# Performance work log

Hardware: AMD Instinct MI355X
Metric: run time of the kernel (lower is better)

The kernel has to match this reference:

```python
import jax, jax.numpy as jnp
import numpy as np

H0, H1, NHID, BATCH = 256, 256, 512, 2048

def setup_inputs() -> dict:
    key = jax.random.key(0)
    k1, k2, k3, k4, k5 = jax.random.split(key, 5)
    initrange = 0.1
    inputs = jax.random.normal(k1, (BATCH, NHID), dtype=jnp.float32)
    labels = jax.random.randint(k2, (BATCH,), 0, H1, dtype=jnp.int32)
    parent_labels = jax.random.randint(k3, (BATCH,), 0, H0, dtype=jnp.int32)
    layer_top_W = jax.random.uniform(k4, (NHID, H0), jnp.float32, -initrange, initrange)
    layer_top_b = jnp.zeros((H0,), jnp.float32)
    layer_bottom_W = jax.random.uniform(k5, (H0, NHID, H1), jnp.float32, -initrange, initrange)
    layer_bottom_b = jnp.zeros((H0, H1), jnp.float32)
    return {"inputs": inputs, "labels": labels, "parent_labels": parent_labels,
            "layer_top_W": layer_top_W, "layer_top_b": layer_top_b,
            "layer_bottom_W": layer_bottom_W, "layer_bottom_b": layer_bottom_b}

def reference(inputs, labels, parent_labels, layer_top_W, layer_top_b,
              layer_bottom_W, layer_bottom_b):
    batch = inputs.shape[0]
    # top-level softmax over coarse classes: [B, H0]
    top_probs = jax.nn.softmax(inputs @ layer_top_W + layer_top_b, axis=1)
    # per-sample gather of expert weight slice [B, NHID, H1] then bmm
    Wb = layer_bottom_W[parent_labels]            # [B, NHID, H1]
    bb = layer_bottom_b[parent_labels]            # [B, H1]
    bottom_logits = jnp.einsum('bd,bdk->bk', inputs, Wb) + bb
    bottom_probs = jax.nn.softmax(bottom_logits, axis=1)
    ar = jnp.arange(batch)
    target_probs = top_probs[ar, parent_labels] * bottom_probs[ar, labels]
    return target_probs
```

## Files before the change

### kernel.cpp

```cpp
#include <hip/hip_runtime.h>

constexpr int BATCH = 2048;
constexpr int NHID  = 512;
constexpr int H0    = 256;
constexpr int H1    = 256;
constexpr int S     = 8;
constexpr int J     = 3;

__global__ __launch_bounds__(128) void hs_8s(
    const float* __restrict__ x,
    const int*   __restrict__ labels,
    const int*   __restrict__ parents,
    const float* __restrict__ topW,
    const float* __restrict__ topb,
    const float* __restrict__ botW,
    const float* __restrict__ botb,
    float*       __restrict__ out)
{
    const int p = blockIdx.x / J;
    const int j = blockIdx.x % J;
    const int t = threadIdx.x;
    const int g = t >> 6;
    const int l = t & 63;

    __shared__ int   list[BATCH];
    __shared__ int   wcnt[2];
    __shared__ __align__(16) float xs[S][NHID];
    __shared__ float psm[2][S];

    int running = 0;
    for (int c = 0; c < BATCH; c += 128) {
        const bool match = (parents[c + t] == p);
        const unsigned long long mask = __ballot(match);
        if (l == 0) wcnt[g] = __popcll(mask);
        __syncthreads();
        const int off = running + (g ? wcnt[0] : 0);
        if (match)
            list[off + __popcll(mask & ((1ull << l) - 1ull))] = c + t;
        running += wcnt[0] + wcnt[1];
        __syncthreads();
    }
    const int n = running;
    if (n <= j * S) return;

    const float* Wbase = g ? botW + (size_t)p * NHID * H1 : topW;
    const float4 b4    = g ? *(const float4*)(botb + (size_t)p * H1 + 4 * l)
                           : *(const float4*)(topb + 4 * l);

    for (int base = j * S; base < n; base += J * S) {
        const int rem = min(S, n - base);

        for (int s = 0; s < S; ++s) {
            const int idx = list[base + min(s, rem - 1)];
            ((float4*)xs[s])[t] = ((const float4*)(x + (size_t)idx * NHID))[t];
        }

        int tgts[S];
        #pragma unroll
        for (int s = 0; s < S; ++s) {
            const int slot = base + min(s, rem - 1);
            tgts[s] = g ? labels[list[slot]] : p;
        }
        __syncthreads();

        float4 acc[S];
        #pragma unroll
        for (int s = 0; s < S; ++s) acc[s] = make_float4(0.f, 0.f, 0.f, 0.f);

        const float* Wp = Wbase + 4 * l;
        float4 ring[8];
        #pragma unroll
        for (int i = 0; i < 8; ++i)
            ring[i] = *(const float4*)(Wp + (size_t)i * H0);

        for (int d = 0; d < NHID; d += 8) {
            #pragma unroll
            for (int h = 0; h < 2; ++h) {
                const int dd = d + 4 * h;
                const float4 w0 = ring[4 * h + 0], w1 = ring[4 * h + 1];
                const float4 w2 = ring[4 * h + 2], w3 = ring[4 * h + 3];
                if (dd + 8 < NHID) {
                    #pragma unroll
                    for (int i = 0; i < 4; ++i)
                        ring[4 * h + i] =
                            *(const float4*)(Wp + (size_t)(dd + 8 + i) * H0);
                }
                #pragma unroll
                for (int s = 0; s < S; ++s) {
                    const float4 xv = *(const float4*)&xs[s][dd];
                    float4 a = acc[s];
                    a.x = fmaf(xv.x, w0.x, a.x); a.y = fmaf(xv.x, w0.y, a.y);
                    a.z = fmaf(xv.x, w0.z, a.z); a.w = fmaf(xv.x, w0.w, a.w);
                    a.x = fmaf(xv.y, w1.x, a.x); a.y = fmaf(xv.y, w1.y, a.y);
                    a.z = fmaf(xv.y, w1.z, a.z); a.w = fmaf(xv.y, w1.w, a.w);
                    a.x = fmaf(xv.z, w2.x, a.x); a.y = fmaf(xv.z, w2.y, a.y);
                    a.z = fmaf(xv.z, w2.z, a.z); a.w = fmaf(xv.z, w2.w, a.w);
                    a.x = fmaf(xv.w, w3.x, a.x); a.y = fmaf(xv.w, w3.y, a.y);
                    a.z = fmaf(xv.w, w3.z, a.z); a.w = fmaf(xv.w, w3.w, a.w);
                    acc[s] = a;
                }
            }
        }

        #pragma unroll
        for (int s = 0; s < S; ++s) {
            float4 v = acc[s];
            v.x += b4.x; v.y += b4.y; v.z += b4.z; v.w += b4.w;

            float m = fmaxf(fmaxf(v.x, v.y), fmaxf(v.z, v.w));
            #pragma unroll
            for (int off = 32; off > 0; off >>= 1)
                m = fmaxf(m, __shfl_xor(m, off, 64));

            const float ex = expf(v.x - m), ey = expf(v.y - m);
            const float ez = expf(v.z - m), ew = expf(v.w - m);
            float sum = (ex + ey) + (ez + ew);
            #pragma unroll
            for (int off = 32; off > 0; off >>= 1)
                sum += __shfl_xor(sum, off, 64);

            const int tgt = tgts[s];
            const int k   = tgt & 3;
            const float ev = (k == 0) ? ex : (k == 1) ? ey : (k == 2) ? ez : ew;
            if (l == (tgt >> 2))
                psm[g][s] = ev / sum;
        }
        __syncthreads();

        if (t < rem) {
            const int idx = list[base + t];
            out[idx] = psm[0][t] * psm[1][t];
        }
        __syncthreads();
    }
}

extern "C" void kernel_launch(void* const* d_in, const int* in_sizes, int n_in,
                              void* d_out, int out_size, void* d_ws, size_t ws_size,
                              hipStream_t stream) {
    const float* x       = (const float*)d_in[0];
    const int*   labels  = (const int*)  d_in[1];
    const int*   parents = (const int*)  d_in[2];
    const float* topW    = (const float*)d_in[3];
    const float* topb    = (const float*)d_in[4];
    const float* botW    = (const float*)d_in[5];
    const float* botb    = (const float*)d_in[6];
    float*       out     = (float*)d_out;

    hs_8s<<<H0 * J, 128, 0, stream>>>(x, labels, parents,
                                      topW, topb, botW, botb, out);
}
```

Baseline: 227.9 us.

## Split output columns across two waves per pass with cross-wave softmax merge

Each block now runs 256 threads: four waves, where each of the top and bottom passes is split across two waves covering 128 output columns each (float2 per lane). Samples per tile rise to 12 and the per-parent split drops from 3 to 2 blocks, so each block re-reads its expert weight slice fewer times in total. Partial max, sum and target-exp values from the two halves are merged in shared memory with a rescaled log-sum-exp. This trades fewer weight re-reads for less per-thread work and more per-wave FMA parallelism, at the cost of extra shuffles, an additional target reduction and more registers for the 12-sample accumulators.

Result: slower. 286.1 us (+25.6%).

```diff
diff --git a/kernel.cpp b/kernel.cpp
--- a/kernel.cpp
+++ b/kernel.cpp
@@ -4,10 +4,10 @@
 constexpr int NHID  = 512;
 constexpr int H0    = 256;
 constexpr int H1    = 256;
-constexpr int S     = 8;
-constexpr int J     = 3;
+constexpr int S     = 12;
+constexpr int NSLOT = 2;
 
-__global__ __launch_bounds__(128) void hs_8s(
+__global__ __launch_bounds__(256) void hs_minbytes(
     const float* __restrict__ x,
     const int*   __restrict__ labels,
     const int*   __restrict__ parents,
@@ -17,119 +17,136 @@
     const float* __restrict__ botb,
     float*       __restrict__ out)
 {
-    const int p = blockIdx.x / J;
-    const int j = blockIdx.x % J;
-    const int t = threadIdx.x;
-    const int g = t >> 6;
-    const int l = t & 63;
+    const int p    = blockIdx.x >> 1;
+    const int slot = blockIdx.x & 1;
+    const int t    = threadIdx.x;
+    const int gb   = t >> 6;
+    const int l    = t & 63;
+    const int mypass = gb >> 1;
+    const int h      = gb & 1;
 
     __shared__ int   list[BATCH];
-    __shared__ int   wcnt[2];
+    __shared__ int   wcnt[4];
     __shared__ __align__(16) float xs[S][NHID];
-    __shared__ float psm[2][S];
+    __shared__ float wm[2][2][S], wsum[2][2][S], wet[2][2][S];
 
     int running = 0;
-    for (int c = 0; c < BATCH; c += 128) {
+    for (int c = 0; c < BATCH; c += 256) {
         const bool match = (parents[c + t] == p);
         const unsigned long long mask = __ballot(match);
-        if (l == 0) wcnt[g] = __popcll(mask);
+        if (l == 0) wcnt[gb] = __popcll(mask);
         __syncthreads();
-        const int off = running + (g ? wcnt[0] : 0);
+        int off = running;
+        for (int w = 0; w < gb; ++w) off += wcnt[w];
         if (match)
             list[off + __popcll(mask & ((1ull << l) - 1ull))] = c + t;
-        running += wcnt[0] + wcnt[1];
+        running += wcnt[0] + wcnt[1] + wcnt[2] + wcnt[3];
         __syncthreads();
     }
     const int n = running;
-    if (n <= j * S) return;
+    if (n <= slot * S) return;
 
-    const float* Wbase = g ? botW + (size_t)p * NHID * H1 : topW;
-    const float4 b4    = g ? *(const float4*)(botb + (size_t)p * H1 + 4 * l)
-                           : *(const float4*)(topb + 4 * l);
+    const float* Wbase = mypass ? botW + (size_t)p * NHID * H1 : topW;
+    const float* Wp    = Wbase + 128 * h + 2 * l;
+    const float2 b2    = mypass
+        ? *(const float2*)(botb + (size_t)p * H1 + 128 * h + 2 * l)
+        : *(const float2*)(topb + 128 * h + 2 * l);
+    const int c0 = 128 * h + 2 * l;
 
-    for (int base = j * S; base < n; base += J * S) {
+    for (int base = slot * S; base < n; base += NSLOT * S) {
         const int rem = min(S, n - base);
 
-        for (int s = 0; s < S; ++s) {
-            const int idx = list[base + min(s, rem - 1)];
-            ((float4*)xs[s])[t] = ((const float4*)(x + (size_t)idx * NHID))[t];
+        for (int pr = 0; pr < S / 2; ++pr) {
+            const int row = 2 * pr + (t >> 7);
+            const int col = t & 127;
+            const int idx = list[base + min(row, rem - 1)];
+            ((float4*)xs[row])[col] = ((const float4*)(x + (size_t)idx * NHID))[col];
         }
 
         int tgts[S];
         #pragma unroll
         for (int s = 0; s < S; ++s) {
-            const int slot = base + min(s, rem - 1);
-            tgts[s] = g ? labels[list[slot]] : p;
+            const int slotidx = base + min(s, rem - 1);
+            tgts[s] = mypass ? labels[list[slotidx]] : p;
         }
         __syncthreads();
 
-        float4 acc[S];
+        float2 acc[S];
         #pragma unroll
-        for (int s = 0; s < S; ++s) acc[s] = make_float4(0.f, 0.f, 0.f, 0.f);
+        for (int s = 0; s < S; ++s) acc[s] = make_float2(0.f, 0.f);
 
-        const float* Wp = Wbase + 4 * l;
-        float4 ring[8];
+        float2 ring[16];
         #pragma unroll
-        for (int i = 0; i < 8; ++i)
-            ring[i] = *(const float4*)(Wp + (size_t)i * H0);
+        for (int i = 0; i < 16; ++i)
+            ring[i] = *(const float2*)(Wp + (size_t)i * H0);
 
-        for (int d = 0; d < NHID; d += 8) {
+        #pragma unroll 4
+        for (int d4 = 0; d4 < NHID / 4; ++d4) {
+            const int rs = (d4 & 3) * 4;
+            const float2 w0 = ring[rs + 0], w1 = ring[rs + 1];
+            const float2 w2 = ring[rs + 2], w3 = ring[rs + 3];
+            const int dn = 4 * d4 + 16;
+            if (dn < NHID) {
+                #pragma unroll
+                for (int i = 0; i < 4; ++i)
+                    ring[rs + i] = *(const float2*)(Wp + (size_t)(dn + i) * H0);
+            }
+            const int d = 4 * d4;
             #pragma unroll
-            for (int h = 0; h < 2; ++h) {
-                const int dd = d + 4 * h;
-                const float4 w0 = ring[4 * h + 0], w1 = ring[4 * h + 1];
-                const float4 w2 = ring[4 * h + 2], w3 = ring[4 * h + 3];
-                if (dd + 8 < NHID) {
-                    #pragma unroll
-                    for (int i = 0; i < 4; ++i)
-                        ring[4 * h + i] =
-                            *(const float4*)(Wp + (size_t)(dd + 8 + i) * H0);
-                }
-                #pragma unroll
-                for (int s = 0; s < S; ++s) {
-                    const float4 xv = *(const float4*)&xs[s][dd];
-                    float4 a = acc[s];
-                    a.x = fmaf(xv.x, w0.x, a.x); a.y = fmaf(xv.x, w0.y, a.y);
-                    a.z = fmaf(xv.x, w0.z, a.z); a.w = fmaf(xv.x, w0.w, a.w);
-                    a.x = fmaf(xv.y, w1.x, a.x); a.y = fmaf(xv.y, w1.y, a.y);
-                    a.z = fmaf(xv.y, w1.z, a.z); a.w = fmaf(xv.y, w1.w, a.w);
-                    a.x = fmaf(xv.z, w2.x, a.x); a.y = fmaf(xv.z, w2.y, a.y);
-                    a.z = fmaf(xv.z, w2.z, a.z); a.w = fmaf(xv.z, w2.w, a.w);
-                    a.x = fmaf(xv.w, w3.x, a.x); a.y = fmaf(xv.w, w3.y, a.y);
-                    a.z = fmaf(xv.w, w3.z, a.z); a.w = fmaf(xv.w, w3.w, a.w);
-                    acc[s] = a;
-                }
+            for (int s = 0; s < S; ++s) {
+                const float4 xv = *(const float4*)&xs[s][d];
+                float2 a = acc[s];
+                a.x = fmaf(xv.x, w0.x, a.x);  a.y = fmaf(xv.x, w0.y, a.y);
+                a.x = fmaf(xv.y, w1.x, a.x);  a.y = fmaf(xv.y, w1.y, a.y);
+                a.x = fmaf(xv.z, w2.x, a.x);  a.y = fmaf(xv.z, w2.y, a.y);
+                a.x = fmaf(xv.w, w3.x, a.x);  a.y = fmaf(xv.w, w3.y, a.y);
+                acc[s] = a;
             }
         }
 
         #pragma unroll
         for (int s = 0; s < S; ++s) {
-            float4 v = acc[s];
-            v.x += b4.x; v.y += b4.y; v.z += b4.z; v.w += b4.w;
+            float2 v = acc[s];
+            v.x += b2.x; v.y += b2.y;
 
-            float m = fmaxf(fmaxf(v.x, v.y), fmaxf(v.z, v.w));
+            float m = fmaxf(v.x, v.y);
             #pragma unroll
             for (int off = 32; off > 0; off >>= 1)
                 m = fmaxf(m, __shfl_xor(m, off, 64));
 
-            const float ex = expf(v.x - m), ey = expf(v.y - m);
-            const float ez = expf(v.z - m), ew = expf(v.w - m);
-            float sum = (ex + ey) + (ez + ew);
+            const float ex = expf(v.x - m);
+            const float ey = expf(v.y - m);
+            float sum = ex + ey;
             #pragma unroll
             for (int off = 32; off > 0; off >>= 1)
                 sum += __shfl_xor(sum, off, 64);
 
             const int tgt = tgts[s];
-            const int k   = tgt & 3;
-            const float ev = (k == 0) ? ex : (k == 1) ? ey : (k == 2) ? ez : ew;
-            if (l == (tgt >> 2))
-                psm[g][s] = ev / sum;
+            float et = (c0 == tgt) ? ex : (c0 + 1 == tgt) ? ey : 0.f;
+            #pragma unroll
+            for (int off = 32; off > 0; off >>= 1)
+                et += __shfl_xor(et, off, 64);
+
+            if (l == 0) {
+                wm[mypass][h][s]   = m;
+                wsum[mypass][h][s] = sum;
+                wet[mypass][h][s]  = et;
+            }
         }
         __syncthreads();
 
         if (t < rem) {
-            const int idx = list[base + t];
-            out[idx] = psm[0][t] * psm[1][t];
+            float pr[2];
+            #pragma unroll
+            for (int ps = 0; ps < 2; ++ps) {
+                const float m0 = wm[ps][0][t], m1 = wm[ps][1][t];
+                const float m  = fmaxf(m0, m1);
+                const float a0 = expf(m0 - m), a1 = expf(m1 - m);
+                const float sum = wsum[ps][0][t] * a0 + wsum[ps][1][t] * a1;
+                const float et  = wet[ps][0][t] * a0 + wet[ps][1][t] * a1;
+                pr[ps] = et / sum;
+            }
+            out[list[base + t]] = pr[0] * pr[1];
         }
         __syncthreads();
     }
@@ -147,6 +164,6 @@
     const float* botb    = (const float*)d_in[6];
     float*       out     = (float*)d_out;
 
-    hs_8s<<<H0 * J, 128, 0, stream>>>(x, labels, parents,
-                                      topW, topb, botW, botb, out);
+    hs_minbytes<<<H0 * NSLOT, 256, 0, stream>>>(x, labels, parents,
+                                                topW, topb, botW, botb, out);
 }
```

## Split into prep, split-K GEMV, and finalize kernels for more parallelism

Applied to the files above, without the earlier changes.

Replaces the single fused kernel with three launches. The first bins samples by parent into a workspace list. The second runs a split-K GEMV over 4 hidden-dimension chunks, with separate blocks for the bottom expert and the top layer, writing partial logits to workspace. The third sums the partials, adds bias and computes both softmax target probabilities. The aim is more blocks, so the per-expert weight stream is spread across more CUs, at the cost of extra launches and a global-memory round trip of partial logits of several MB.

Measured after the change: 245.0 us. 7.5% more time.

```diff
diff --git a/kernel.cpp b/kernel.cpp
--- a/kernel.cpp
+++ b/kernel.cpp
@@ -4,135 +4,168 @@
 constexpr int NHID  = 512;
 constexpr int H0    = 256;
 constexpr int H1    = 256;
-constexpr int S     = 8;
-constexpr int J     = 3;
+constexpr int KCH   = 4;
+constexpr int DCH   = NHID / KCH;
+constexpr int S     = 16;
+constexpr int LSTRIDE = 2048;
+constexpr int NBOT  = H0 * KCH;
+constexpr int NTOP  = (BATCH / S) * KCH;
 
-__global__ __launch_bounds__(128) void hs_8s(
-    const float* __restrict__ x,
-    const int*   __restrict__ labels,
-    const int*   __restrict__ parents,
-    const float* __restrict__ topW,
-    const float* __restrict__ topb,
-    const float* __restrict__ botW,
-    const float* __restrict__ botb,
-    float*       __restrict__ out)
-{
-    const int p = blockIdx.x / J;
-    const int j = blockIdx.x % J;
-    const int t = threadIdx.x;
-    const int g = t >> 6;
-    const int l = t & 63;
 
-    __shared__ int   list[BATCH];
-    __shared__ int   wcnt[2];
-    __shared__ __align__(16) float xs[S][NHID];
-    __shared__ float psm[2][S];
-
+__global__ __launch_bounds__(256) void k_prep(const int* __restrict__ parents,
+                                              int* __restrict__ list,
+                                              int* __restrict__ nval) {
+    const int p = blockIdx.x, t = threadIdx.x, g = t >> 6, l = t & 63;
+    __shared__ int wcnt[4];
     int running = 0;
-    for (int c = 0; c < BATCH; c += 128) {
+    for (int c = 0; c < BATCH; c += 256) {
         const bool match = (parents[c + t] == p);
         const unsigned long long mask = __ballot(match);
         if (l == 0) wcnt[g] = __popcll(mask);
         __syncthreads();
-        const int off = running + (g ? wcnt[0] : 0);
+        int off = running;
+        for (int w = 0; w < g; ++w) off += wcnt[w];
         if (match)
-            list[off + __popcll(mask & ((1ull << l) - 1ull))] = c + t;
-        running += wcnt[0] + wcnt[1];
+            list[p * LSTRIDE + off + __popcll(mask & ((1ull << l) - 1ull))] = c + t;
+        running += wcnt[0] + wcnt[1] + wcnt[2] + wcnt[3];
         __syncthreads();
     }
-    const int n = running;
-    if (n <= j * S) return;
+    if (t == 0) nval[p] = running;
+}
 
-    const float* Wbase = g ? botW + (size_t)p * NHID * H1 : topW;
-    const float4 b4    = g ? *(const float4*)(botb + (size_t)p * H1 + 4 * l)
-                           : *(const float4*)(topb + 4 * l);
+__device__ __forceinline__ void gemv_tile(const float* __restrict__ Wp,
+                                          const float xs[S][DCH],
+                                          float4 acc[S]) {
+    float4 ring[8];
+    #pragma unroll
+    for (int i = 0; i < 8; ++i)
+        ring[i] = *(const float4*)(Wp + (size_t)i * 256);
 
-    for (int base = j * S; base < n; base += J * S) {
-        const int rem = min(S, n - base);
+    for (int d = 0; d < DCH; d += 8) {
+        #pragma unroll
+        for (int h = 0; h < 2; ++h) {
+            const int dd = d + 4 * h;
+            const float4 w0 = ring[4 * h + 0], w1 = ring[4 * h + 1];
+            const float4 w2 = ring[4 * h + 2], w3 = ring[4 * h + 3];
+            if (dd + 8 < DCH) {
+                #pragma unroll
+                for (int i = 0; i < 4; ++i)
+                    ring[4 * h + i] =
+                        *(const float4*)(Wp + (size_t)(dd + 8 + i) * 256);
+            }
+            #pragma unroll
+            for (int s = 0; s < S; ++s) {
+                const float4 xv = *(const float4*)&xs[s][dd];
+                float4 a = acc[s];
+                a.x = fmaf(xv.x, w0.x, a.x); a.y = fmaf(xv.x, w0.y, a.y);
+                a.z = fmaf(xv.x, w0.z, a.z); a.w = fmaf(xv.x, w0.w, a.w);
+                a.x = fmaf(xv.y, w1.x, a.x); a.y = fmaf(xv.y, w1.y, a.y);
+                a.z = fmaf(xv.y, w1.z, a.z); a.w = fmaf(xv.y, w1.w, a.w);
+                a.x = fmaf(xv.z, w2.x, a.x); a.y = fmaf(xv.z, w2.y, a.y);
+                a.z = fmaf(xv.z, w2.z, a.z); a.w = fmaf(xv.z, w2.w, a.w);
+                a.x = fmaf(xv.w, w3.x, a.x); a.y = fmaf(xv.w, w3.y, a.y);
+                a.z = fmaf(xv.w, w3.z, a.z); a.w = fmaf(xv.w, w3.w, a.w);
+                acc[s] = a;
+            }
+        }
+    }
+}
 
-        for (int s = 0; s < S; ++s) {
-            const int idx = list[base + min(s, rem - 1)];
-            ((float4*)xs[s])[t] = ((const float4*)(x + (size_t)idx * NHID))[t];
+__global__ __launch_bounds__(64) void k_gemv(
+    const float* __restrict__ x, const float* __restrict__ topW,
+    const float* __restrict__ botW, const int* __restrict__ list,
+    const int* __restrict__ nval, float* __restrict__ wstop,
+    float* __restrict__ wsbot) {
+    const int b = blockIdx.x, l = threadIdx.x;
+    __shared__ __align__(16) float xs[S][DCH];
+    __shared__ int sid[S];
+
+    if (b < NBOT) {
+        const int p = b >> 2, k = b & 3;
+        const int n = nval[p];
+        const float* W = botW + ((size_t)p * NHID + (size_t)k * DCH) * H1 + 4 * l;
+        for (int tb = 0; tb < n; tb += S) {
+            const int rem = min(S, n - tb);
+            for (int i = l; i < S; i += 64)
+                sid[i] = list[p * LSTRIDE + tb + min(i, rem - 1)];
+            __syncthreads();
+            for (int i = l; i < S * (DCH / 4); i += 64) {
+                const int s = i >> 5, c = i & 31;
+                ((float4*)xs[s])[c] =
+                    *(const float4*)(x + (size_t)sid[s] * NHID + k * DCH + 4 * c);
+            }
+            __syncthreads();
+            float4 acc[S];
+            #pragma unroll
+            for (int s = 0; s < S; ++s) acc[s] = make_float4(0.f, 0.f, 0.f, 0.f);
+            gemv_tile(W, xs, acc);
+            for (int s = 0; s < rem; ++s)
+                *(float4*)(wsbot + ((size_t)sid[s] * KCH + k) * H1 + 4 * l) = acc[s];
+            __syncthreads();
         }
-
-        int tgts[S];
-        #pragma unroll
-        for (int s = 0; s < S; ++s) {
-            const int slot = base + min(s, rem - 1);
-            tgts[s] = g ? labels[list[slot]] : p;
+    } else {
+        const int bb = b - NBOT, j = bb >> 2, k = bb & 3;
+        const float* W = topW + (size_t)k * DCH * H0 + 4 * l;
+        for (int i = l; i < S * (DCH / 4); i += 64) {
+            const int s = i >> 5, c = i & 31;
+            ((float4*)xs[s])[c] =
+                *(const float4*)(x + (size_t)(S * j + s) * NHID + k * DCH + 4 * c);
         }
         __syncthreads();
-
         float4 acc[S];
         #pragma unroll
         for (int s = 0; s < S; ++s) acc[s] = make_float4(0.f, 0.f, 0.f, 0.f);
+        gemv_tile(W, xs, acc);
+        #pragma unroll
+        for (int s = 0; s < S; ++s)
+            *(float4*)(wstop + ((size_t)(S * j + s) * KCH + k) * H0 + 4 * l) = acc[s];
+    }
+}
 
-        const float* Wp = Wbase + 4 * l;
-        float4 ring[8];
+__global__ __launch_bounds__(64) void k_fin(
+    const int* __restrict__ labels, const int* __restrict__ parents,
+    const float* __restrict__ topb, const float* __restrict__ botb,
+    const float* __restrict__ wstop, const float* __restrict__ wsbot,
+    float* __restrict__ out) {
+    const int s = blockIdx.x, l = threadIdx.x;
+    const int par = parents[s];
+    float pr[2];
+    #pragma unroll
+    for (int pass = 0; pass < 2; ++pass) {
+        const float* wsrc = pass ? wsbot : wstop;
+        float4 v = make_float4(0.f, 0.f, 0.f, 0.f);
         #pragma unroll
-        for (int i = 0; i < 8; ++i)
-            ring[i] = *(const float4*)(Wp + (size_t)i * H0);
+        for (int k = 0; k < KCH; ++k) {
+            const float4 c = *(const float4*)(wsrc + ((size_t)s * KCH + k) * 256 + 4 * l);
+            v.x += c.x; v.y += c.y; v.z += c.z; v.w += c.w;
+        }
+        const float4 bias = pass ? *(const float4*)(botb + (size_t)par * H1 + 4 * l)
+                                 : *(const float4*)(topb + 4 * l);
+        v.x += bias.x; v.y += bias.y; v.z += bias.z; v.w += bias.w;
 
-        for (int d = 0; d < NHID; d += 8) {
-            #pragma unroll
-            for (int h = 0; h < 2; ++h) {
-                const int dd = d + 4 * h;
-                const float4 w0 = ring[4 * h + 0], w1 = ring[4 * h + 1];
-                const float4 w2 = ring[4 * h + 2], w3 = ring[4 * h + 3];
-                if (dd + 8 < NHID) {
-                    #pragma unroll
-                    for (int i = 0; i < 4; ++i)
-                        ring[4 * h + i] =
-                            *(const float4*)(Wp + (size_t)(dd + 8 + i) * H0);
-                }
-                #pragma unroll
-                for (int s = 0; s < S; ++s) {
-                    const float4 xv = *(const float4*)&xs[s][dd];
-                    float4 a = acc[s];
-                    a.x = fmaf(xv.x, w0.x, a.x); a.y = fmaf(xv.x, w0.y, a.y);
-                    a.z = fmaf(xv.x, w0.z, a.z); a.w = fmaf(xv.x, w0.w, a.w);
-                    a.x = fmaf(xv.y, w1.x, a.x); a.y = fmaf(xv.y, w1.y, a.y);
-                    a.z = fmaf(xv.y, w1.z, a.z); a.w = fmaf(xv.y, w1.w, a.w);
-                    a.x = fmaf(xv.z, w2.x, a.x); a.y = fmaf(xv.z, w2.y, a.y);
-                    a.z = fmaf(xv.z, w2.z, a.z); a.w = fmaf(xv.z, w2.w, a.w);
-                    a.x = fmaf(xv.w, w3.x, a.x); a.y = fmaf(xv.w, w3.y, a.y);
-                    a.z = fmaf(xv.w, w3.z, a.z); a.w = fmaf(xv.w, w3.w, a.w);
-                    acc[s] = a;
-                }
-            }
-        }
+        float m = fmaxf(fmaxf(v.x, v.y), fmaxf(v.z, v.w));
+        #pragma unroll
+        for (int off = 32; off > 0; off >>= 1)
+            m = fmaxf(m, __shfl_xor(m, off, 64));
 
+        const float ex = expf(v.x - m), ey = expf(v.y - m);
+        const float ez = expf(v.z - m), ew = expf(v.w - m);
+        float sum = (ex + ey) + (ez + ew);
         #pragma unroll
-        for (int s = 0; s < S; ++s) {
-            float4 v = acc[s];
-            v.x += b4.x; v.y += b4.y; v.z += b4.z; v.w += b4.w;
+        for (int off = 32; off > 0; off >>= 1)
+            sum += __shfl_xor(sum, off, 64);
 
-            float m = fmaxf(fmaxf(v.x, v.y), fmaxf(v.z, v.w));
-            #pragma unroll
-            for (int off = 32; off > 0; off >>= 1)
-                m = fmaxf(m, __shfl_xor(m, off, 64));
+        const int tgt = pass ? labels[s] : par;
+        const int c0 = 4 * l;
+        float et = (c0 == tgt) ? ex : (c0 + 1 == tgt) ? ey
+                 : (c0 + 2 == tgt) ? ez : (c0 + 3 == tgt) ? ew : 0.f;
+        #pragma unroll
+        for (int off = 32; off > 0; off >>= 1)
+            et += __shfl_xor(et, off, 64);
 
-            const float ex = expf(v.x - m), ey = expf(v.y - m);
-            const float ez = expf(v.z - m), ew = expf(v.w - m);
-            float sum = (ex + ey) + (ez + ew);
-            #pragma unroll
-            for (int off = 32; off > 0; off >>= 1)
-                sum += __shfl_xor(sum, off, 64);
-
-            const int tgt = tgts[s];
-            const int k   = tgt & 3;
-            const float ev = (k == 0) ? ex : (k == 1) ? ey : (k == 2) ? ez : ew;
-            if (l == (tgt >> 2))
-                psm[g][s] = ev / sum;
-        }
-        __syncthreads();
-
-        if (t < rem) {
-            const int idx = list[base + t];
-            out[idx] = psm[0][t] * psm[1][t];
-        }
-        __syncthreads();
+        pr[pass] = et / sum;
     }
+    if (l == 0) out[s] = pr[0] * pr[1];
 }
 
 extern "C" void kernel_launch(void* const* d_in, const int* in_sizes, int n_in,
@@ -147,6 +180,12 @@
     const float* botb    = (const float*)d_in[6];
     float*       out     = (float*)d_out;
 
-    hs_8s<<<H0 * J, 128, 0, stream>>>(x, labels, parents,
-                                      topW, topb, botW, botb, out);
+    int*   list  = (int*)d_ws;
+    int*   nval  = (int*)((char*)d_ws + (size_t)H0 * LSTRIDE * sizeof(int));
+    float* wstop = (float*)((char*)d_ws + (size_t)H0 * LSTRIDE * sizeof(int) + 4096);
+    float* wsbot = wstop + (size_t)BATCH * KCH * H0;
+
+    k_prep<<<H0, 256, 0, stream>>>(parents, list, nval);
+    k_gemv<<<NBOT + NTOP, 64, 0, stream>>>(x, topW, botW, list, nval, wstop, wsbot);
+    k_fin<<<BATCH, 64, 0, stream>>>(labels, parents, topb, botb, wstop, wsbot, out);
 }
```
